# Kernel tuning notes

Measured on AMD Instinct MI355X. Metric: run time of the kernel, lower is better.

Reference implementation:

```python
import jax, jax.numpy as jnp
import numpy as np

EPS = 1e-08


def setup_inputs() -> dict:
    key = jax.random.key(0)
    k1, = jax.random.split(key, 1)
    B, T, F = 64, 1000, 257
    mag = jax.random.uniform(k1, (B, T, F), dtype=jnp.float32)
    s = jnp.zeros((B, F), dtype=jnp.float32)
    weights = jnp.ones((1, 1, F), dtype=jnp.float32)
    bias = jnp.zeros((1, 1, F), dtype=jnp.float32)
    alpha = jnp.full((1, F), -4.0, dtype=jnp.float32)
    return {"mag": mag, "s": s, "weights": weights, "bias": bias, "alpha": alpha}


def reference(mag, s, weights, bias, alpha):
    # mag: [B, T, F]; s: [B, F] initial EMA state
    power = mag * mag                      # [B, T, F]
    a = jax.nn.sigmoid(alpha)              # [1, F], broadcasts over B

    def step(carry, p_t):
        # carry: [B, F], p_t: [B, F]
        new = carry * (1.0 - a) + p_t * a
        return new, new

    # scan over time axis: move T to leading axis
    _, smooth = jax.lax.scan(step, s, jnp.swapaxes(power, 0, 1))  # smooth: [T, B, F]
    smooth_data = jnp.sqrt(jnp.swapaxes(smooth, 0, 1))            # [B, T, F]
    return mag / (smooth_data + EPS) * weights + bias
```

## Files before the change

### kernel.cpp

```cpp
#include <hip/hip_runtime.h>

#define EPS 1e-8f


template <int L>
__global__ __launch_bounds__(256)
void fns4_aggregate(const float* __restrict__ mag,
                    const float* __restrict__ alpha,
                    float* __restrict__ S,
                    int B, int T, int F, int C) {
    const int BF = B * F;
    int g = blockIdx.x * blockDim.x + threadIdx.x;
    if (g >= BF * C) return;
    const int bf = g % BF;
    const int c  = g / BF;
    const int b  = bf / F;
    const int f  = bf - b * F;

    const float a   = 1.0f / (1.0f + expf(-alpha[f]));
    const float oma = 1.0f - a;

    const float* p = mag + ((size_t)b * T + (size_t)c * L) * F + f;

    float local = 0.0f;
#pragma unroll
    for (int t = 0; t < L; ++t) {
        float m = p[(size_t)t * F];
        local = local * oma + (m * m) * a;
    }
    S[(size_t)c * BF + bf] = local;
}

template <int L>
__global__ __launch_bounds__(256)
void fns4_emit(const float* __restrict__ mag,
               const float* __restrict__ s0,
               const float* __restrict__ weights,
               const float* __restrict__ bias,
               const float* __restrict__ alpha,
               const float* __restrict__ S,
               float* __restrict__ out,
               int B, int T, int F, int C) {
    const int BF = B * F;
    int g = blockIdx.x * blockDim.x + threadIdx.x;
    if (g >= BF * C) return;
    const int bf = g % BF;
    const int c  = g / BF;
    const int b  = bf / F;
    const int f  = bf - b * F;

    const float a   = 1.0f / (1.0f + expf(-alpha[f]));
    const float oma = 1.0f - a;
    const float w   = weights[f];
    const float bi  = bias[f];

    float carry = s0[bf];
    if (c > 0) {
        const float D = powf(oma, (float)L);
        for (int j = 0; j < c; ++j)
            carry = carry * D + S[(size_t)j * BF + bf];
    }

    const float* p = mag + ((size_t)b * T + (size_t)c * L) * F + f;
    float*       o = out + ((size_t)b * T + (size_t)c * L) * F + f;

#pragma unroll
    for (int t = 0; t < L; ++t) {
        float m = p[(size_t)t * F];
        carry = carry * oma + (m * m) * a;
        o[(size_t)t * F] = m / (sqrtf(carry) + EPS) * w + bi;
    }
}

__global__ void fns4_fallback(const float* __restrict__ mag,
                              const float* __restrict__ s0,
                              const float* __restrict__ weights,
                              const float* __restrict__ bias,
                              const float* __restrict__ alpha,
                              float* __restrict__ out,
                              int B, int T, int F) {
    int bf = blockIdx.x * blockDim.x + threadIdx.x;
    int BF = B * F;
    if (bf >= BF) return;
    int b = bf / F;
    int f = bf - b * F;

    float a  = 1.0f / (1.0f + expf(-alpha[f]));
    float w  = weights[f];
    float bi = bias[f];

    float carry = s0[bf];
    const float* p = mag + (size_t)b * T * F + f;
    float*       o = out + (size_t)b * T * F + f;

    for (int t = 0; t < T; ++t) {
        float m = p[(size_t)t * F];
        carry = carry * (1.0f - a) + (m * m) * a;
        o[(size_t)t * F] = m / (sqrtf(carry) + EPS) * w + bi;
    }
}

extern "C" void kernel_launch(void* const* d_in, const int* in_sizes, int n_in,
                              void* d_out, int out_size, void* d_ws, size_t ws_size,
                              hipStream_t stream) {
    const float* mag     = (const float*)d_in[0];
    const float* s0      = (const float*)d_in[1];
    const float* weights = (const float*)d_in[2];
    const float* bias    = (const float*)d_in[3];
    const float* alpha   = (const float*)d_in[4];
    float* out = (float*)d_out;

    int F  = in_sizes[4];
    int BF = in_sizes[1];
    int B  = BF / F;
    int T  = in_sizes[0] / BF;

    constexpr int L = 50;
    if (T % L == 0) {
        int C = T / L;
        size_t need = (size_t)C * BF * sizeof(float);
        if (ws_size >= need) {
            float* S = (float*)d_ws;
            int total  = BF * C;
            int blocks = (total + 255) / 256;
            fns4_aggregate<L><<<blocks, 256, 0, stream>>>(
                mag, alpha, S, B, T, F, C);
            fns4_emit<L><<<blocks, 256, 0, stream>>>(
                mag, s0, weights, bias, alpha, S, out, B, T, F, C);
            return;
        }
    }

    int threads = 256;
    int blocks  = (BF + threads - 1) / threads;
    fns4_fallback<<<blocks, threads, 0, stream>>>(mag, s0, weights, bias,
                                                  alpha, out, B, T, F);
}
```

Before: 46.64 us.

## Skip last-chunk aggregate, use rcp and nontemporal stores, partially unroll loops

The aggregate pass no longer computes the final chunk's summary, because emit never reads it. This removes about one twentieth of the first-pass reads. The emit loop replaces the division with a hardware reciprocal and writes output with nontemporal stores to reduce cache pollution. Both loops drop full unrolling for unroll-by-10, and powf is replaced by repeated multiplication. The reciprocal may lose some precision compared with a true division.

```diff
diff --git a/kernel.cpp b/kernel.cpp
--- a/kernel.cpp
+++ b/kernel.cpp
@@ -5,13 +5,13 @@
 
 template <int L>
 __global__ __launch_bounds__(256)
-void fns4_aggregate(const float* __restrict__ mag,
+void fns6_aggregate(const float* __restrict__ mag,
                     const float* __restrict__ alpha,
                     float* __restrict__ S,
-                    int B, int T, int F, int C) {
+                    int B, int T, int F, int C1) {
     const int BF = B * F;
     int g = blockIdx.x * blockDim.x + threadIdx.x;
-    if (g >= BF * C) return;
+    if (g >= BF * C1) return;
     const int bf = g % BF;
     const int c  = g / BF;
     const int b  = bf / F;
@@ -23,7 +23,7 @@
     const float* p = mag + ((size_t)b * T + (size_t)c * L) * F + f;
 
     float local = 0.0f;
-#pragma unroll
+#pragma unroll 10
     for (int t = 0; t < L; ++t) {
         float m = p[(size_t)t * F];
         local = local * oma + (m * m) * a;
@@ -33,7 +33,7 @@
 
 template <int L>
 __global__ __launch_bounds__(256)
-void fns4_emit(const float* __restrict__ mag,
+void fns6_emit(const float* __restrict__ mag,
                const float* __restrict__ s0,
                const float* __restrict__ weights,
                const float* __restrict__ bias,
@@ -56,7 +56,9 @@
 
     float carry = s0[bf];
     if (c > 0) {
-        const float D = powf(oma, (float)L);
+        float D = 1.0f;
+#pragma unroll
+        for (int i = 0; i < L; ++i) D *= oma;
         for (int j = 0; j < c; ++j)
             carry = carry * D + S[(size_t)j * BF + bf];
     }
@@ -64,21 +66,23 @@
     const float* p = mag + ((size_t)b * T + (size_t)c * L) * F + f;
     float*       o = out + ((size_t)b * T + (size_t)c * L) * F + f;
 
-#pragma unroll
+#pragma unroll 10
     for (int t = 0; t < L; ++t) {
         float m = p[(size_t)t * F];
         carry = carry * oma + (m * m) * a;
-        o[(size_t)t * F] = m / (sqrtf(carry) + EPS) * w + bi;
+        float r = __builtin_amdgcn_rcpf(sqrtf(carry) + EPS);
+        float v = m * r * w + bi;
+        __builtin_nontemporal_store(v, o + (size_t)t * F);
     }
 }
 
-__global__ void fns4_fallback(const float* __restrict__ mag,
-                              const float* __restrict__ s0,
-                              const float* __restrict__ weights,
-                              const float* __restrict__ bias,
-                              const float* __restrict__ alpha,
-                              float* __restrict__ out,
-                              int B, int T, int F) {
+__global__ void fns_fallback(const float* __restrict__ mag,
+                             const float* __restrict__ s0,
+                             const float* __restrict__ weights,
+                             const float* __restrict__ bias,
+                             const float* __restrict__ alpha,
+                             float* __restrict__ out,
+                             int B, int T, int F) {
     int bf = blockIdx.x * blockDim.x + threadIdx.x;
     int BF = B * F;
     if (bf >= BF) return;
@@ -117,15 +121,17 @@
 
     constexpr int L = 50;
     if (T % L == 0) {
-        int C = T / L;
-        size_t need = (size_t)C * BF * sizeof(float);
-        if (ws_size >= need) {
+        int C  = T / L;
+        int C1 = C - 1;
+        size_t need = (size_t)C1 * BF * sizeof(float);
+        if (C1 >= 1 && ws_size >= need) {
             float* S = (float*)d_ws;
-            int total  = BF * C;
-            int blocks = (total + 255) / 256;
-            fns4_aggregate<L><<<blocks, 256, 0, stream>>>(
-                mag, alpha, S, B, T, F, C);
-            fns4_emit<L><<<blocks, 256, 0, stream>>>(
+
+            int n1 = BF * C1;
+            int n2 = BF * C;
+            fns6_aggregate<L><<<(n1 + 255) / 256, 256, 0, stream>>>(
+                mag, alpha, S, B, T, F, C1);
+            fns6_emit<L><<<(n2 + 255) / 256, 256, 0, stream>>>(
                 mag, s0, weights, bias, alpha, S, out, B, T, F, C);
             return;
         }
@@ -133,6 +139,6 @@
 
     int threads = 256;
     int blocks  = (BF + threads - 1) / threads;
-    fns4_fallback<<<blocks, threads, 0, stream>>>(mag, s0, weights, bias,
-                                                  alpha, out, B, T, F);
+    fns_fallback<<<blocks, threads, 0, stream>>>(mag, s0, weights, bias,
+                                                 alpha, out, B, T, F);
 }
```

Result: slower. 49.80 us (+6.8%).
